# Kernel optimization log

Hardware: AMD Instinct MI355X
Metric: run time of the kernel (lower is better)

Reference implementation:

```python
import jax, jax.numpy as jnp
import numpy as np
import math

B, T, D, H = 4, 2048, 512, 8
MAX_LEN = 2048
DK = D // H


def setup_inputs() -> dict:
    key = jax.random.key(0)
    ks = jax.random.split(key, 12)
    s = 0.02
    inp = {
        "x": jax.random.normal(ks[0], (B, T, D), dtype=jnp.float32),
        "mask": jax.random.bernoulli(ks[1], 0.85, (B, T)),  # True = observed
        "Wq": jax.random.normal(ks[2], (D, D), dtype=jnp.float32) * s,
        "bq": jnp.zeros((D,), dtype=jnp.float32),
        "Wk": jax.random.normal(ks[3], (D, D), dtype=jnp.float32) * s,
        "bk": jnp.zeros((D,), dtype=jnp.float32),
        "Wv": jax.random.normal(ks[4], (D, D), dtype=jnp.float32) * s,
        "bv": jnp.zeros((D,), dtype=jnp.float32),
        "Wo": jax.random.normal(ks[5], (D, D), dtype=jnp.float32) * s,
        "bo": jnp.zeros((D,), dtype=jnp.float32),
        "missing_bias": jnp.zeros((1, H, 1, 1), dtype=jnp.float32),
        "rel_pos_embed": jax.random.normal(ks[6], (2 * MAX_LEN - 1, H), dtype=jnp.float32) * 0.01,
    }
    return inp


def _sinusoidal_pe(t, d):
    pos = jnp.arange(t, dtype=jnp.float32)[:, None]                      # [T,1]
    div = jnp.exp(jnp.arange(0, d, 2, dtype=jnp.float32) * (-math.log(10000.0) / d))
    pe = jnp.zeros((t, d), dtype=jnp.float32)
    pe = pe.at[:, 0::2].set(jnp.sin(pos * div))
    pe = pe.at[:, 1::2].set(jnp.cos(pos * div))
    return pe


def _attention(x, mask, Wq, bq, Wk, bk, Wv, bv, Wo, bo, missing_bias, rel_pos_embed):
    b, t, d = x.shape
    h = missing_bias.shape[1]
    dk = d // h
    max_len = (rel_pos_embed.shape[0] + 1) // 2

    x = x + _sinusoidal_pe(t, d)[None]

    def proj(w, bias):  # [B,T,D] -> [B,H,T,dk]
        y = jnp.einsum('btd,ed->bte', x, w) + bias
        return y.reshape(b, t, h, dk).transpose(0, 2, 1, 3)

    Q, K, V = proj(Wq, bq), proj(Wk, bk), proj(Wv, bv)

    scores = jnp.einsum('bhqd,bhkd->bhqk', Q, K) / math.sqrt(dk)  # [B,H,T,T]

    # relative position bias, antisymmetrized
    pos = jnp.arange(t)
    rel_idx = pos[:, None] - pos[None, :] + (max_len - 1)          # [T,T]
    bias = rel_pos_embed[rel_idx]                                  # [T,T,H]
    bias = 0.5 * (bias - bias.transpose(1, 0, 2))
    scores = scores + bias.transpose(2, 0, 1)[None]                # [B,H,T,T]

    # missing-token masking on keys: -inf fill then add missing_bias at masked spots
    m = mask[:, None, None, :]                                     # [B,1,1,T]
    scores = jnp.where(m, scores, -jnp.inf)
    scores = jnp.where(m, scores, scores + missing_bias)

    attn = jax.nn.softmax(scores, axis=-1)
    out = jnp.einsum('bhqk,bhkd->bhqd', attn, V)
    out = out.transpose(0, 2, 1, 3).reshape(b, t, d)
    return jnp.einsum('btd,ed->bte', out, Wo) + bo


def reference(x, mask, Wq, bq, Wk, bk, Wv, bv, Wo, bo, missing_bias, rel_pos_embed):
    return _attention(x, mask, Wq, bq, Wk, bk, Wv, bv, Wo, bo, missing_bias, rel_pos_embed)
```

## Files before the change

kernel.cpp:

```cpp
#include <hip/hip_runtime.h>

#define B_ 4
#define T_ 2048
#define D_ 512
#define H_ 8
#define DK_ 64
#define TBL 4095

typedef __attribute__((ext_vector_type(4))) float f32x4;
typedef __attribute__((ext_vector_type(8))) short bf16x8;
typedef __attribute__((ext_vector_type(4))) int i32x4;
typedef unsigned int u32;

static __device__ __forceinline__ float b2f(ushort u) {
    union { float f; unsigned int i; } c;
    c.i = ((unsigned int)u) << 16;
    return c.f;
}

static __device__ __forceinline__ ushort f2b(float f) {
    union { float f; unsigned int i; } c;
    c.f = f;
    unsigned int i = c.i;
    unsigned int r = (i + 0x7fffu + ((i >> 16) & 1u)) >> 16;
    return (ushort)r;
}

static __device__ __forceinline__ void gload_lds16(const void* g, void* l) {
    __builtin_amdgcn_global_load_lds(
        (const __attribute__((address_space(1))) u32*)g,
        (__attribute__((address_space(3))) u32*)(u32)(unsigned long long)l,
        16, 0, 0);
}

__global__ __launch_bounds__(64) void detect_mask_kernel(const unsigned int* __restrict__ mask,
                                                         int* __restrict__ flags) {
    int lane = threadIdx.x;
    int c2 = 0, c1 = 0;
    for (int i = lane; i < 512; i += 64) {
        unsigned int v = mask[i];
        c2 += (v == 0x3F803F80u || v == 0x00010001u) ? 1 : 0;
        c1 += (v == 0x01010101u) ? 1 : 0;
    }
#pragma unroll
    for (int m = 1; m < 64; m <<= 1) {
        c2 += __shfl_xor(c2, m);
        c1 += __shfl_xor(c1, m);
    }
    if (lane == 0) flags[0] = (c2 > 8) ? 2 : ((c1 > 8) ? 1 : 0);
}

__global__ __launch_bounds__(256) void mask_prep_kernel(const void* __restrict__ mask,
                                                        const int* __restrict__ flags,
                                                        int* __restrict__ maskw) {
    int j = blockIdx.x * 256 + threadIdx.x;
    int fm = flags[0];
    int v;
    if (fm == 2)      v = (((const ushort*)mask)[j] != 0);
    else if (fm == 1) v = (((const unsigned char*)mask)[j] != 0);
    else              v = (((const int*)mask)[j] != 0);
    maskw[j] = v;
}

__global__ __launch_bounds__(256) void wcvt_kernel(
    const float* __restrict__ W0, const float* __restrict__ W1,
    const float* __restrict__ W2, const float* __restrict__ W3,
    ushort* __restrict__ Wc) {
    const int z = blockIdx.z;
    const float* Ws = (z == 0) ? W0 : ((z == 1) ? W1 : ((z == 2) ? W2 : W3));
    int idx = blockIdx.x * 256 + threadIdx.x;
    const float* wf = Ws + idx * 8;
    f32x4 a = *(const f32x4*)(wf);
    f32x4 c = *(const f32x4*)(wf + 4);
    union { ushort u[8]; i32x4 v; } o;
#pragma unroll
    for (int j = 0; j < 4; ++j) { o.u[j] = f2b(a[j]); o.u[4 + j] = f2b(c[j]); }
    *(i32x4*)(Wc + (size_t)z * (D_ * D_) + idx * 8) = o.v;
}

__global__ __launch_bounds__(256) void pe_kernel(const float* __restrict__ x,
                                                 ushort* __restrict__ xp) {
    int idx = blockIdx.x * 256 + threadIdx.x;
    int i = idx & 255;
    int row = idx >> 8;
    int t = row & (T_ - 1);
    float div = __expf((float)i * -0.035977892f);
    float ang = (float)t * div;
    float s = sinf(ang);
    float c = cosf(ang);
    float2 v = ((const float2*)x)[row * 256 + i];
    unsigned int o = (unsigned int)f2b(v.x + s) | ((unsigned int)f2b(v.y + c) << 16);
    *(unsigned int*)(xp + (size_t)row * D_ + 2 * i) = o;
}

__global__ __launch_bounds__(256) void bias_tbl_kernel(const float* __restrict__ E,
                                                       float* __restrict__ tbl) {
    int idx = blockIdx.x * 256 + threadIdx.x;
    if (idx >= TBL * H_) return;
    int h = idx & 7;
    int j = idx >> 3;
    tbl[(size_t)h * TBL + j] =
        0.72134752044f * (E[(size_t)j * H_ + h] - E[(size_t)(4094 - j) * H_ + h]);
}

template <int OUTMODE>
__global__ __launch_bounds__(256) void gemm_bt_kernel(
    const ushort* __restrict__ A,
    const ushort* __restrict__ W0, const ushort* __restrict__ W1, const ushort* __restrict__ W2,
    const float* __restrict__ bias0, const float* __restrict__ bias1, const float* __restrict__ bias2,
    void* __restrict__ O0, void* __restrict__ O1, void* __restrict__ O2) {
    __shared__ ushort As[128 * 64];
    __shared__ ushort Bs[128 * 64];

    const int z = blockIdx.z;
    const ushort* Wp = (z == 0) ? W0 : ((z == 1) ? W1 : W2);
    const float* bp = (z == 0) ? bias0 : ((z == 1) ? bias1 : bias2);
    void* Op = (z == 0) ? O0 : ((z == 1) ? O1 : O2);

    const int n0 = blockIdx.x * 128;
    const int m0 = blockIdx.y * 128;
    const int tid = threadIdx.x;
    const int lane = tid & 63;
    const int w = tid >> 6;
    const int wr = (w >> 1) * 64;
    const int wc = (w & 1) * 64;
    const int l15 = lane & 15;
    const int lg = lane >> 4;

    f32x4 acc[4][4];
#pragma unroll
    for (int mi = 0; mi < 4; ++mi)
#pragma unroll
        for (int ni = 0; ni < 4; ++ni)
            acc[mi][ni] = (f32x4){0.f, 0.f, 0.f, 0.f};

    for (int kt = 0; kt < D_ / 64; ++kt) {
#pragma unroll
        for (int p = 0; p < 4; ++p) {
            int c = tid + p * 256;
            int r = c >> 3;
            int scol = ((c & 7) ^ (r & 7)) * 8;
            gload_lds16(A  + (size_t)(m0 + r) * D_ + kt * 64 + scol, As + c * 8);
            gload_lds16(Wp + (size_t)(n0 + r) * D_ + kt * 64 + scol, Bs + c * 8);
        }
        __syncthreads();

#pragma unroll
        for (int ks = 0; ks < 2; ++ks) {
            bf16x8 af[4], bfr[4];
#pragma unroll
            for (int mi = 0; mi < 4; ++mi)
                af[mi] = *(const bf16x8*)(As + (wr + mi * 16 + l15) * 64 +
                                          (((ks * 4 + lg) ^ (l15 & 7)) * 8));
#pragma unroll
            for (int ni = 0; ni < 4; ++ni)
                bfr[ni] = *(const bf16x8*)(Bs + (wc + ni * 16 + l15) * 64 +
                                           (((ks * 4 + lg) ^ (l15 & 7)) * 8));
#pragma unroll
            for (int mi = 0; mi < 4; ++mi)
#pragma unroll
                for (int ni = 0; ni < 4; ++ni)
                    acc[mi][ni] = __builtin_amdgcn_mfma_f32_16x16x32_bf16(af[mi], bfr[ni], acc[mi][ni], 0, 0, 0);
        }
        __syncthreads();
    }

#pragma unroll
    for (int ni = 0; ni < 4; ++ni) {
        int n = n0 + wc + ni * 16 + l15;
        float bv = bp[n];
#pragma unroll
        for (int mi = 0; mi < 4; ++mi) {
#pragma unroll
            for (int i = 0; i < 4; ++i) {
                int m = m0 + wr + mi * 16 + lg * 4 + i;
                float v = acc[mi][ni][i] + bv;
                if (OUTMODE == 0) {
                    int b = m >> 11;
                    int t = m & 2047;
                    int hh = n >> 6;
                    int dk = n & 63;
                    size_t off;
                    if (z == 2) off = ((size_t)(b * H_ + hh) * DK_ + dk) * T_ + t;
                    else        off = (((size_t)(b * H_ + hh) * T_ + t) << 6) + dk;
                    ((ushort*)Op)[off] = f2b(v);
                } else {
                    ((float*)Op)[(size_t)m * D_ + n] = v;
                }
            }
        }
    }
}

__global__ __launch_bounds__(512) void attn_kernel(
    const ushort* __restrict__ Q, const ushort* __restrict__ K, const ushort* __restrict__ Vt,
    const int* __restrict__ maskw, const float* __restrict__ tbl,
    ushort* __restrict__ Aout) {
    __shared__ ushort Ks[64 * 64];
    __shared__ ushort Vs[64 * 64];
    __shared__ ushort Ps[8][16 * 64];
    __shared__ float biasl[2176];
    __shared__ ushort maskl[T_];

    const int qb = blockIdx.x;
    const int bh = blockIdx.y;
    const int b = bh >> 3;
    const int h = bh & 7;
    const int tid = threadIdx.x;
    const int lane = tid & 63;
    const int w = tid >> 6;
    const int l15 = lane & 15;
    const int lg = lane >> 4;

    const ushort* Qp = Q + (size_t)bh * T_ * DK_;
    const ushort* Kp = K + (size_t)bh * T_ * DK_;
    const ushort* Vp = Vt + (size_t)bh * DK_ * T_;

    for (int j = tid; j < 2176; j += 512) {
        int gj = qb * 128 + j;
        biasl[j] = (gj <= 4094) ? tbl[(size_t)h * TBL + gj] : 0.f;
    }
    for (int j = tid; j < T_; j += 512)
        maskl[j] = (maskw[b * T_ + j] != 0) ? 0x3F80 : 0;

    const int q0 = qb * 128 + w * 16;
    bf16x8 qf[2];
#pragma unroll
    for (int kf = 0; kf < 2; ++kf)
        qf[kf] = *(const bf16x8*)(Qp + (size_t)(q0 + l15) * DK_ + kf * 32 + lg * 8);

    f32x4 acc[4];
    float rs[4];
#pragma unroll
    for (int ni = 0; ni < 4; ++ni) acc[ni] = (f32x4){0.f, 0.f, 0.f, 0.f};
#pragma unroll
    for (int i = 0; i < 4; ++i) rs[i] = 0.f;
    __syncthreads();

    for (int kt = 0; kt < T_ / 64; ++kt) {
        {
            int r = tid >> 3;
            int scol = ((tid & 7) ^ (r & 7)) * 8;
            gload_lds16(Kp + (size_t)(kt * 64 + r) * DK_ + scol, Ks + tid * 8);
            gload_lds16(Vp + (size_t)r * T_ + kt * 64 + scol, Vs + tid * 8);
        }
        __syncthreads();

#pragma unroll
        for (int ct = 0; ct < 4; ++ct) {
            int krow = ct * 16 + l15;
            bf16x8 kf0 = *(const bf16x8*)(Ks + krow * 64 + ((lg ^ (krow & 7)) * 8));
            bf16x8 kf1 = *(const bf16x8*)(Ks + krow * 64 + (((4 + lg) ^ (krow & 7)) * 8));
            int kg = kt * 64 + ct * 16 + l15;
            float mf = b2f(maskl[kg]);
            f32x4 S = (f32x4){0.f, 0.f, 0.f, 0.f};
            S = __builtin_amdgcn_mfma_f32_16x16x32_bf16(qf[0], kf0, S, 0, 0, 0);
            S = __builtin_amdgcn_mfma_f32_16x16x32_bf16(qf[1], kf1, S, 0, 0, 0);
            int jb = w * 16 + lg * 4 - kg + 2047;
#pragma unroll
            for (int i = 0; i < 4; ++i) {
                float pv = mf * exp2f(fmaf(S[i], 0.1803368801f, biasl[jb + i]));
                rs[i] += pv;
                int prow = lg * 4 + i;
                int pcol = ct * 16 + l15;
                Ps[w][prow * 64 + (((pcol >> 3) ^ (prow & 7)) * 8) + (pcol & 7)] = f2b(pv);
            }
        }

#pragma unroll
        for (int kk = 0; kk < 2; ++kk) {
            bf16x8 pf = *(const bf16x8*)(Ps[w] + l15 * 64 + (((kk * 4 + lg) ^ (l15 & 7)) * 8));
#pragma unroll
            for (int ni = 0; ni < 4; ++ni) {
                int vrow = ni * 16 + l15;
                bf16x8 vf = *(const bf16x8*)(Vs + vrow * 64 + (((kk * 4 + lg) ^ (vrow & 7)) * 8));
                acc[ni] = __builtin_amdgcn_mfma_f32_16x16x32_bf16(pf, vf, acc[ni], 0, 0, 0);
            }
        }
        __syncthreads();
    }

#pragma unroll
    for (int i = 0; i < 4; ++i) {
        float v = rs[i];
        v += __shfl_xor(v, 1);
        v += __shfl_xor(v, 2);
        v += __shfl_xor(v, 4);
        v += __shfl_xor(v, 8);
        rs[i] = v;
    }

#pragma unroll
    for (int ni = 0; ni < 4; ++ni)
#pragma unroll
        for (int i = 0; i < 4; ++i) {
            int t = q0 + lg * 4 + i;
            int d = h * DK_ + ni * 16 + l15;
            Aout[(size_t)(b * T_ + t) * D_ + d] = f2b(acc[ni][i] / rs[i]);
        }
}

extern "C" void kernel_launch(void* const* d_in, const int* in_sizes, int n_in,
                              void* d_out, int out_size, void* d_ws, size_t ws_size,
                              hipStream_t stream) {
    const float* x   = (const float*)d_in[0];
    const void* mask = d_in[1];
    const float* Wq  = (const float*)d_in[2];
    const float* bq  = (const float*)d_in[3];
    const float* Wk  = (const float*)d_in[4];
    const float* bk  = (const float*)d_in[5];
    const float* Wv  = (const float*)d_in[6];
    const float* bv  = (const float*)d_in[7];
    const float* Wo  = (const float*)d_in[8];
    const float* bo  = (const float*)d_in[9];
    const float* E   = (const float*)d_in[11];
    float* out = (float*)d_out;

    char* ws = (char*)d_ws;
    ushort* xp  = (ushort*)(ws);
    ushort* Qw  = (ushort*)(ws + (8u << 20));
    ushort* Kw  = (ushort*)(ws + (16u << 20));
    ushort* Vw  = (ushort*)(ws + (24u << 20));
    float* tbl  = (float*)(ws + (32u << 20));
    ushort* Wc  = (ushort*)(ws + (32u << 20) + 262144);
    int* maskw  = (int*)(ws + (34u << 20) + 262144);
    int* flags  = (int*)(ws + (34u << 20) + 262144 + 32768);

    if (ws_size < (35u << 20)) return;

    detect_mask_kernel<<<1, 64, 0, stream>>>((const unsigned int*)mask, flags);
    mask_prep_kernel<<<(B_ * T_) / 256, 256, 0, stream>>>(mask, flags, maskw);
    bias_tbl_kernel<<<(TBL * H_ + 255) / 256, 256, 0, stream>>>(E, tbl);
    pe_kernel<<<B_ * T_, 256, 0, stream>>>(x, xp);

    dim3 gw(128, 1, 4);
    wcvt_kernel<<<gw, 256, 0, stream>>>(Wq, Wk, Wv, Wo, Wc);

    dim3 g1(D_ / 128, (B_ * T_) / 128, 3);
    gemm_bt_kernel<0><<<g1, 256, 0, stream>>>(xp, Wc, Wc + D_ * D_, Wc + 2 * D_ * D_,
                                              bq, bk, bv, Qw, Kw, Vw);

    dim3 g2(T_ / 128, B_ * H_, 1);
    attn_kernel<<<g2, 512, 0, stream>>>(Qw, Kw, Vw, maskw, tbl, xp);

    dim3 g3(D_ / 128, (B_ * T_) / 128, 1);
    gemm_bt_kernel<1><<<g3, 256, 0, stream>>>(xp, Wc + 3 * D_ * D_, Wc + 3 * D_ * D_, Wc + 3 * D_ * D_,
                                              bo, bo, bo, out, out, out);
}
```

Measured before the change: 231.1 us.

## Stage V-transpose stores via LDS, transpose QK MFMA, additive mask, remap attention grid

The QKV GEMM now writes the transposed V output through an LDS staging buffer, so global stores are coalesced 16-byte vectors instead of scattered 2-byte writes. In the attention kernel the QK^T MFMA operands are swapped so each lane holds one query row across four keys. The mask becomes an additive -1e5 term loaded as a float4, P is packed with v_cvt_pk_bf16_f32, and the row-sum reduction shrinks to two shuffles plus an LDS exchange. The attention grid is also flattened to a 1D launch with a remapped block order, likely for better L2 and XCD locality of K/V. Together these cut VALU work and store inefficiency, at the cost of an extra barrier and relying on exp2 underflow to zero out masked keys.

```diff
diff --git a/kernel.cpp b/kernel.cpp
--- a/kernel.cpp
+++ b/kernel.cpp
@@ -109,8 +109,9 @@
     const ushort* __restrict__ W0, const ushort* __restrict__ W1, const ushort* __restrict__ W2,
     const float* __restrict__ bias0, const float* __restrict__ bias1, const float* __restrict__ bias2,
     void* __restrict__ O0, void* __restrict__ O1, void* __restrict__ O2) {
-    __shared__ ushort As[128 * 64];
-    __shared__ ushort Bs[128 * 64];
+    __shared__ ushort SBUF[128 * 136];
+    ushort* As = SBUF;
+    ushort* Bs = SBUF + 128 * 64;
 
     const int z = blockIdx.z;
     const ushort* Wp = (z == 0) ? W0 : ((z == 1) ? W1 : W2);
@@ -165,27 +166,47 @@
         __syncthreads();
     }
 
-#pragma unroll
-    for (int ni = 0; ni < 4; ++ni) {
-        int n = n0 + wc + ni * 16 + l15;
-        float bv = bp[n];
-#pragma unroll
-        for (int mi = 0; mi < 4; ++mi) {
-#pragma unroll
-            for (int i = 0; i < 4; ++i) {
-                int m = m0 + wr + mi * 16 + lg * 4 + i;
-                float v = acc[mi][ni][i] + bv;
-                if (OUTMODE == 0) {
-                    int b = m >> 11;
-                    int t = m & 2047;
-                    int hh = n >> 6;
-                    int dk = n & 63;
-                    size_t off;
-                    if (z == 2) off = ((size_t)(b * H_ + hh) * DK_ + dk) * T_ + t;
-                    else        off = (((size_t)(b * H_ + hh) * T_ + t) << 6) + dk;
-                    ((ushort*)Op)[off] = f2b(v);
-                } else {
-                    ((float*)Op)[(size_t)m * D_ + n] = v;
+    if (OUTMODE == 0 && z == 2) {
+#pragma unroll
+        for (int ni = 0; ni < 4; ++ni) {
+            int nl = wc + ni * 16 + l15;
+            float bv = bp[n0 + nl];
+#pragma unroll
+            for (int mi = 0; mi < 4; ++mi)
+#pragma unroll
+                for (int i = 0; i < 4; ++i)
+                    SBUF[nl * 136 + wr + mi * 16 + lg * 4 + i] = f2b(acc[mi][ni][i] + bv);
+        }
+        __syncthreads();
+        const int bb = m0 >> 11;
+        const int t0 = m0 & 2047;
+#pragma unroll
+        for (int it = 0; it < 8; ++it) {
+            int cc = it * 256 + tid;
+            int nl = cc >> 4;
+            int mc = cc & 15;
+            int n = n0 + nl;
+            size_t off = ((size_t)(bb * H_ + (n >> 6)) * DK_ + (n & 63)) * T_ + t0 + mc * 8;
+            *(i32x4*)((ushort*)Op + off) = *(const i32x4*)(SBUF + nl * 136 + mc * 8);
+        }
+    } else {
+#pragma unroll
+        for (int ni = 0; ni < 4; ++ni) {
+            int n = n0 + wc + ni * 16 + l15;
+            float bv = bp[n];
+#pragma unroll
+            for (int mi = 0; mi < 4; ++mi) {
+#pragma unroll
+                for (int i = 0; i < 4; ++i) {
+                    int m = m0 + wr + mi * 16 + lg * 4 + i;
+                    float v = acc[mi][ni][i] + bv;
+                    if (OUTMODE == 0) {
+                        int b = m >> 11;
+                        int t = m & 2047;
+                        ((ushort*)Op)[(((size_t)(b * H_ + (n >> 6)) * T_ + t) << 6) + (n & 63)] = f2b(v);
+                    } else {
+                        ((float*)Op)[(size_t)m * D_ + n] = v;
+                    }
                 }
             }
         }
@@ -200,10 +221,12 @@
     __shared__ ushort Vs[64 * 64];
     __shared__ ushort Ps[8][16 * 64];
     __shared__ float biasl[2176];
-    __shared__ ushort maskl[T_];
-
-    const int qb = blockIdx.x;
-    const int bh = blockIdx.y;
+    __shared__ float maskf[T_];
+
+    const int id = blockIdx.x;
+    const int j1 = id >> 3;
+    const int bh = (id & 7) * 4 + (j1 >> 4);
+    const int qb = j1 & 15;
     const int b = bh >> 3;
     const int h = bh & 7;
     const int tid = threadIdx.x;
@@ -221,7 +244,7 @@
         biasl[j] = (gj <= 4094) ? tbl[(size_t)h * TBL + gj] : 0.f;
     }
     for (int j = tid; j < T_; j += 512)
-        maskl[j] = (maskw[b * T_ + j] != 0) ? 0x3F80 : 0;
+        maskf[j] = (maskw[b * T_ + j] != 0) ? 0.f : -100000.f;
 
     const int q0 = qb * 128 + w * 16;
     bf16x8 qf[2];
@@ -230,12 +253,14 @@
         qf[kf] = *(const bf16x8*)(Qp + (size_t)(q0 + l15) * DK_ + kf * 32 + lg * 8);
 
     f32x4 acc[4];
-    float rs[4];
+    float rs = 0.f;
 #pragma unroll
     for (int ni = 0; ni < 4; ++ni) acc[ni] = (f32x4){0.f, 0.f, 0.f, 0.f};
-#pragma unroll
-    for (int i = 0; i < 4; ++i) rs[i] = 0.f;
     __syncthreads();
+
+    char* PsB = (char*)Ps[w];
+    const u32 prow = (u32)(l15 * 128);
+    const u32 pxor = (u32)(l15 & 7);
 
     for (int kt = 0; kt < T_ / 64; ++kt) {
         {
@@ -251,25 +276,29 @@
             int krow = ct * 16 + l15;
             bf16x8 kf0 = *(const bf16x8*)(Ks + krow * 64 + ((lg ^ (krow & 7)) * 8));
             bf16x8 kf1 = *(const bf16x8*)(Ks + krow * 64 + (((4 + lg) ^ (krow & 7)) * 8));
-            int kg = kt * 64 + ct * 16 + l15;
-            float mf = b2f(maskl[kg]);
             f32x4 S = (f32x4){0.f, 0.f, 0.f, 0.f};
-            S = __builtin_amdgcn_mfma_f32_16x16x32_bf16(qf[0], kf0, S, 0, 0, 0);
-            S = __builtin_amdgcn_mfma_f32_16x16x32_bf16(qf[1], kf1, S, 0, 0, 0);
-            int jb = w * 16 + lg * 4 - kg + 2047;
-#pragma unroll
-            for (int i = 0; i < 4; ++i) {
-                float pv = mf * exp2f(fmaf(S[i], 0.1803368801f, biasl[jb + i]));
-                rs[i] += pv;
-                int prow = lg * 4 + i;
-                int pcol = ct * 16 + l15;
-                Ps[w][prow * 64 + (((pcol >> 3) ^ (prow & 7)) * 8) + (pcol & 7)] = f2b(pv);
-            }
+            S = __builtin_amdgcn_mfma_f32_16x16x32_bf16(kf0, qf[0], S, 0, 0, 0);
+            S = __builtin_amdgcn_mfma_f32_16x16x32_bf16(kf1, qf[1], S, 0, 0, 0);
+            int k0 = ct * 16 + lg * 4;
+            f32x4 mv = *(const f32x4*)(maskf + kt * 64 + k0);
+            int jb0 = w * 16 + l15 - (kt * 64 + k0) + 2047;
+            float p0 = exp2f(fmaf(S[0], 0.1803368801f, biasl[jb0]     + mv[0]));
+            float p1 = exp2f(fmaf(S[1], 0.1803368801f, biasl[jb0 - 1] + mv[1]));
+            float p2 = exp2f(fmaf(S[2], 0.1803368801f, biasl[jb0 - 2] + mv[2]));
+            float p3 = exp2f(fmaf(S[3], 0.1803368801f, biasl[jb0 - 3] + mv[3]));
+            rs += (p0 + p1) + (p2 + p3);
+            u32 pk0, pk1;
+            asm("v_cvt_pk_bf16_f32 %0, %1, %2" : "=v"(pk0) : "v"(p0), "v"(p1));
+            asm("v_cvt_pk_bf16_f32 %0, %1, %2" : "=v"(pk1) : "v"(p2), "v"(p3));
+            u32 slot16 = (u32)(ct * 2 + (lg >> 1));
+            u32 byte0 = prow + ((slot16 ^ pxor) << 4) + (u32)((lg & 1) * 8);
+            *(u32*)(PsB + byte0) = pk0;
+            *(u32*)(PsB + byte0 + 4) = pk1;
         }
 
 #pragma unroll
         for (int kk = 0; kk < 2; ++kk) {
-            bf16x8 pf = *(const bf16x8*)(Ps[w] + l15 * 64 + (((kk * 4 + lg) ^ (l15 & 7)) * 8));
+            bf16x8 pf = *(const bf16x8*)(PsB + prow + ((((u32)(kk * 4 + lg)) ^ pxor) << 4));
 #pragma unroll
             for (int ni = 0; ni < 4; ++ni) {
                 int vrow = ni * 16 + l15;
@@ -280,15 +309,11 @@
         __syncthreads();
     }
 
-#pragma unroll
-    for (int i = 0; i < 4; ++i) {
-        float v = rs[i];
-        v += __shfl_xor(v, 1);
-        v += __shfl_xor(v, 2);
-        v += __shfl_xor(v, 4);
-        v += __shfl_xor(v, 8);
-        rs[i] = v;
-    }
+    rs += __shfl_xor(rs, 16);
+    rs += __shfl_xor(rs, 32);
+    float* rsl = (float*)Ks;
+    if (lane < 16) rsl[w * 16 + lane] = rs;
+    __syncthreads();
 
 #pragma unroll
     for (int ni = 0; ni < 4; ++ni)
@@ -296,7 +321,7 @@
         for (int i = 0; i < 4; ++i) {
             int t = q0 + lg * 4 + i;
             int d = h * DK_ + ni * 16 + l15;
-            Aout[(size_t)(b * T_ + t) * D_ + d] = f2b(acc[ni][i] / rs[i]);
+            Aout[(size_t)(b * T_ + t) * D_ + d] = f2b(acc[ni][i] / rsl[w * 16 + lg * 4 + i]);
         }
 }
 
@@ -340,8 +365,7 @@
     gemm_bt_kernel<0><<<g1, 256, 0, stream>>>(xp, Wc, Wc + D_ * D_, Wc + 2 * D_ * D_,
                                               bq, bk, bv, Qw, Kw, Vw);
 
-    dim3 g2(T_ / 128, B_ * H_, 1);
-    attn_kernel<<<g2, 512, 0, stream>>>(Qw, Kw, Vw, maskw, tbl, xp);
+    attn_kernel<<<512, 512, 0, stream>>>(Qw, Kw, Vw, maskw, tbl, xp);
 
     dim3 g3(D_ / 128, (B_ * T_) / 128, 1);
     gemm_bt_kernel<1><<<g3, 256, 0, stream>>>(xp, Wc + 3 * D_ * D_, Wc + 3 * D_ * D_, Wc + 3 * D_ * D_,
```

Measured after the change: 220.6 us. -4.6%, faster.
